# Kernel tuning notes

Measured on AMD Instinct MI355X. Metric: run time of the kernel, lower is better.

## Reference

```python
import jax, jax.numpy as jnp
import numpy as np

N = 64      # SSM state size (hidden_size)
H = 1024    # channels
L = 2048    # sequence length
BATCH = 8


def setup_inputs() -> dict:
    key = jax.random.key(0)
    ks = jax.random.split(key, 12)
    s = 1.0 / np.sqrt(N)
    n = jnp.arange(N, dtype=jnp.float32)
    return {
        "r": jax.random.normal(ks[0], (BATCH, L, H), dtype=jnp.float32),
        "B_re": jax.random.normal(ks[1], (N,), dtype=jnp.float32) * s,
        "B_im": jax.random.normal(ks[2], (N,), dtype=jnp.float32) * s,
        "C_re": jax.random.normal(ks[3], (H, N), dtype=jnp.float32) * s,
        "C_im": jax.random.normal(ks[4], (H, N), dtype=jnp.float32) * s,
        "P_re": jax.random.normal(ks[5], (N,), dtype=jnp.float32) * s,
        "P_im": jax.random.normal(ks[6], (N,), dtype=jnp.float32) * s,
        "Q_re": jax.random.normal(ks[7], (N,), dtype=jnp.float32) * s,
        "Q_im": jax.random.normal(ks[8], (N,), dtype=jnp.float32) * s,
        # HiPPO-LegS-like diagonal: negative real part for stability, imag ~ pi*n
        "diag_re": -0.5 * jnp.ones((N,), dtype=jnp.float32),
        "diag_im": jnp.pi * (n - N / 2.0),
        "step": jnp.array([1e-3], dtype=jnp.float32),
        "D": jnp.zeros((1,), dtype=jnp.float32),
    }


def _dplr_kernel(Bc, Cc, Pc, Qc, Lam, step, seq_len):
    # Standard S4 DPLR generating function evaluated at roots of unity,
    # then inverse FFT -> real convolution kernel K_c of shape (H, L).
    z = jnp.exp(-2j * jnp.pi * jnp.arange(seq_len) / seq_len).astype(jnp.complex64)  # (L,)
    g = (2.0 / step) * (1.0 - z) / (1.0 + z)                                          # (L,)
    cden = 1.0 / (g[:, None] - Lam[None, :])                                          # (L,N) Cauchy denom
    k00 = jnp.einsum('hn,ln->hl', Cc * Bc, cden)   # (H,L)
    k01 = jnp.einsum('hn,ln->hl', Cc * Pc, cden)   # (H,L)
    k10 = jnp.einsum('n,ln->l', Qc * Bc, cden)     # (L,)
    k11 = jnp.einsum('n,ln->l', Qc * Pc, cden)     # (L,)
    at_roots = (2.0 / (1.0 + z)) * (k00 - k01 * (k10 / (1.0 + k11)))  # (H,L)
    return jnp.fft.ifft(at_roots, axis=-1).real


def reference(r, B_re, B_im, C_re, C_im, P_re, P_im, Q_re, Q_im,
              diag_re, diag_im, step, D):
    step_c = jnp.maximum(step[0], 1e-6)
    Bc = B_re + 1j * B_im
    Cc = C_re + 1j * C_im
    Pc = P_re + 1j * P_im
    Qc = Q_re + 1j * Q_im
    Lam = diag_re + 1j * diag_im
    seq_len = r.shape[1]
    K = _dplr_kernel(Bc, Cc, Pc, Qc, Lam, step_c, seq_len)  # (H, L)
    # causal FFT convolution along the sequence axis
    nfft = 2 * seq_len
    Kf = jnp.fft.rfft(K, n=nfft, axis=-1)            # (H, nfft//2+1)
    uf = jnp.fft.rfft(r, n=nfft, axis=1)             # (B, nfft//2+1, H)
    h1 = jnp.fft.irfft(uf * Kf.T[None], n=nfft, axis=1)[:, :seq_len]  # (B,L,H)
    y1 = h1 + D[0] * r
    return jax.nn.gelu(y1, approximate=False)
```

## Files before the change

kernel.cpp:

```cpp
#include <hip/hip_runtime.h>
#include <math.h>

#define SSM_N 64
#define SSM_H 1024
#define SSM_L 2048
#define SSM_B 8
#define FFTN 2048
#define NT 256

#define PSWZ(a) ((a) ^ (((a) >> 4) & 15))

typedef float f2 __attribute__((ext_vector_type(2)));
static __device__ __forceinline__ f2 mkf2(float a, float b){ f2 v; v.x = a; v.y = b; return v; }

static __device__ __forceinline__ f2 cmul(f2 a, f2 b){
  return mkf2(-a.y, a.y) * mkf2(b.y, b.x) + mkf2(a.x, a.x) * b;
}
static __device__ __forceinline__ f2 cconj(f2 a){ return mkf2(a.x, -a.y); }

template<bool INV> static __device__ __forceinline__ f2 mul_mi(f2 a){
  return INV ? mkf2(-a.y, a.x) : mkf2(a.y, -a.x);
}
template<bool INV> static __device__ __forceinline__ f2 mul_w81(f2 a){
  const float r = 0.70710678118654752440f;
  return INV ? (r * mkf2(a.x - a.y, a.y + a.x)) : (r * mkf2(a.x + a.y, a.y - a.x));
}
template<bool INV> static __device__ __forceinline__ f2 mul_w83(f2 a){
  const float r = 0.70710678118654752440f;
  return INV ? (r * mkf2(-(a.x + a.y), a.x - a.y)) : (r * mkf2(a.y - a.x, -(a.x + a.y)));
}

#define W8C0 1.f
#define W8S0 0.f
#define W8C1 0.92387953251f
#define W8S1 (-0.38268343236f)
#define W8C2 0.70710678119f
#define W8S2 (-0.70710678119f)
#define W8C3 0.38268343236f
#define W8S3 (-0.92387953251f)
#define W8C4 0.f
#define W8S4 (-1.f)
#define W8C5 (-0.38268343236f)
#define W8S5 (-0.92387953251f)
#define W8C6 (-0.70710678119f)
#define W8S6 (-0.70710678119f)
#define W8C7 (-0.92387953251f)
#define W8S7 (-0.38268343236f)

template<bool INV>
static __device__ __forceinline__ void bfly8(const f2* x, f2* y)
{
  f2 t0=x[0]+x[4], t4=x[0]-x[4];
  f2 t1=x[1]+x[5], t5=x[1]-x[5];
  f2 t2=x[2]+x[6], t6=x[2]-x[6];
  f2 t3=x[3]+x[7], t7=x[3]-x[7];
  f2 b0=t0+t2, b2=t0-t2, b1=t1+t3, b3=t1-t3;
  f2 mb3 = mul_mi<INV>(b3);
  y[0]=b0+b1; y[4]=b0-b1; y[2]=b2+mb3; y[6]=b2-mb3;
  f2 v1 = mul_w81<INV>(t5), v2 = mul_mi<INV>(t6), v3 = mul_w83<INV>(t7);
  f2 a0=t4+v2, a2=t4-v2, a1=v1+v3, a3=v1-v3;
  f2 ma3 = mul_mi<INV>(a3);
  y[1]=a0+a1; y[5]=a0-a1; y[3]=a2+ma3; y[7]=a2-ma3;
}

template<bool INV>
static __device__ __forceinline__ void calc_w8(const f2* __restrict__ tw, int j, f2* w)
{
  f2 w1 = tw[j];
  if (INV) w1.y = -w1.y;
  w[1]=w1; w[2]=cmul(w1,w1); w[3]=cmul(w[2],w1); w[4]=cmul(w[2],w[2]);
  w[5]=cmul(w[3],w[2]); w[6]=cmul(w[3],w[3]); w[7]=cmul(w[4],w[3]);
}

static __device__ __forceinline__ void twstore(f2* __restrict__ dst, const f2* y, const f2* w,
                                               int base, int S)
{
  dst[PSWZ(base)]     = y[0];
  dst[PSWZ(base+S)]   = cmul(y[1],w[1]);
  dst[PSWZ(base+2*S)] = cmul(y[2],w[2]);
  dst[PSWZ(base+3*S)] = cmul(y[3],w[3]);
  dst[PSWZ(base+4*S)] = cmul(y[4],w[4]);
  dst[PSWZ(base+5*S)] = cmul(y[5],w[5]);
  dst[PSWZ(base+6*S)] = cmul(y[6],w[6]);
  dst[PSWZ(base+7*S)] = cmul(y[7],w[7]);
}

template<bool INV>
static __device__ __forceinline__ void bfly8_store(f2* __restrict__ dst, const f2* __restrict__ tw,
                                                   f2* x, int j, int base, int S)
{
  f2 y[8]; bfly8<INV>(x, y);
  f2 w[8]; calc_w8<INV>(tw, j, w);
  twstore(dst, y, w, base, S);
}

template<bool INV, int S>
static __device__ __forceinline__ void stage8_mid_ip(f2* __restrict__ buf, const f2* __restrict__ tw,
                                                     int t, int st)
{
  f2 x[8];
  #pragma unroll
  for (int q = 0; q < 8; ++q) x[q] = buf[st + 256*q];
  __syncthreads();
  int i = t & (S-1);
  int j = t - i;
  bfly8_store<INV>(buf, tw, x, j, i + j*8, S);
  __syncthreads();
}

template<bool INV>
static __device__ __forceinline__ void stage4f_ip(f2* __restrict__ buf, int st)
{
  f2 xr[2][4];
  #pragma unroll
  for (int hh = 0; hh < 2; ++hh) {
    const f2* sp = buf + st + 256*hh;
    xr[hh][0]=sp[0]; xr[hh][1]=sp[512]; xr[hh][2]=sp[1024]; xr[hh][3]=sp[1536];
  }
  __syncthreads();
  #pragma unroll
  for (int hh = 0; hh < 2; ++hh) {
    f2* wp = buf + st + 256*hh;
    f2 a0=xr[hh][0]+xr[hh][2], a2=xr[hh][0]-xr[hh][2];
    f2 a1=xr[hh][1]+xr[hh][3], a3=xr[hh][1]-xr[hh][3];
    f2 m = mul_mi<INV>(a3);
    wp[0]    = a0+a1;
    wp[512]  = a2+m;
    wp[1024] = a0-a1;
    wp[1536] = a2-m;
  }
  __syncthreads();
}

template<bool INV>
static __device__ __forceinline__ void stage4f_reg(const f2* __restrict__ src, f2* out, int st)
{
  #pragma unroll
  for (int hh = 0; hh < 2; ++hh) {
    const f2* sp = src + st + 256*hh;
    f2 x0=sp[0], x1=sp[512], x2=sp[1024], x3=sp[1536];
    f2 a0=x0+x2, a2=x0-x2, a1=x1+x3, a3=x1-x3;
    f2 m = mul_mi<INV>(a3);
    out[hh]   = a0+a1;
    out[hh+2] = a2+m;
    out[hh+4] = a0-a1;
    out[hh+6] = a2-m;
  }
}

static __device__ __forceinline__ f2 init_tw(f2* tw, int t)
{
  float s, c;
  sincosf(-6.2831853071795864769f * (float)t / (float)FFTN, &s, &c);
  f2 v = mkf2(c, s);
  tw[t] = v;
  return v;
}

__global__ __launch_bounds__(256) void kprep(
    const float* __restrict__ B_re, const float* __restrict__ B_im,
    const float* __restrict__ P_re, const float* __restrict__ P_im,
    const float* __restrict__ Q_re, const float* __restrict__ Q_im,
    const float* __restrict__ diag_re, const float* __restrict__ diag_im,
    const float* __restrict__ step,
    f2* __restrict__ cdenT, f2* __restrict__ f2v, f2* __restrict__ facv)
{
  int gid = blockIdx.x * 256 + threadIdx.x;
  int l = gid >> 3, s = gid & 7;
  double stepc = (double)step[0]; if (stepc < 1e-6) stepc = 1e-6;
  double ang = -2.0 * 3.14159265358979323846 * (double)l / (double)SSM_L;
  double zr = cos(ang), zi = sin(ang);
  double dr = 1.0 + zr, di = zi;
  double nr = 1.0 - zr, ni = -zi;
  double den = dr*dr + di*di;
  double i2s = 2.0 / stepc;
  double gr = i2s * (nr*dr + ni*di) / den;
  double gi = i2s * (ni*dr - nr*di) / den;
  double k10r=0.0, k10i=0.0, k11r=0.0, k11i=0.0;
  #pragma unroll
  for (int q = 0; q < 8; ++q) {
    int n = s*8 + q;
    double ar = gr - (double)diag_re[n];
    double ai = gi - (double)diag_im[n];
    double d2 = ar*ar + ai*ai;
    double cr = ar/d2, ci = -ai/d2;
    cdenT[n*SSM_L + l] = mkf2((float)cr, (float)ci);
    double qr = (double)Q_re[n], qi = (double)Q_im[n];
    double br = (double)B_re[n], bi = (double)B_im[n];
    double pr = (double)P_re[n], pi = (double)P_im[n];
    double qbr = qr*br - qi*bi, qbi = qr*bi + qi*br;
    double qpr = qr*pr - qi*pi, qpi = qr*pi + qi*pr;
    k10r += qbr*cr - qbi*ci; k10i += qbr*ci + qbi*cr;
    k11r += qpr*cr - qpi*ci; k11i += qpr*ci + qpi*cr;
  }
  #pragma unroll
  for (int off = 1; off < 8; off <<= 1) {
    k10r += __shfl_xor(k10r, off);
    k10i += __shfl_xor(k10i, off);
    k11r += __shfl_xor(k11r, off);
    k11i += __shfl_xor(k11i, off);
  }
  if (s == 0) {
    f2v[l] = mkf2((float)(2.0*dr/den), (float)(-2.0*di/den));
    double er = 1.0 + k11r, ei = k11i;
    double ed = er*er + ei*ei;
    facv[l] = mkf2((float)((k10r*er + k10i*ei)/ed), (float)((k10i*er - k10r*ei)/ed));
  }
}

__global__ __launch_bounds__(NT, 3) void kmid(
    const float* __restrict__ r, float* __restrict__ rT,
    const float* __restrict__ C_re, const float* __restrict__ C_im,
    const float* __restrict__ B_re, const float* __restrict__ B_im,
    const float* __restrict__ P_re, const float* __restrict__ P_im,
    const f2* __restrict__ cdenT, const f2* __restrict__ f2v, const f2* __restrict__ facv,
    float4* __restrict__ PQg)
{
  __shared__ f2 smem[FFTN + 256];
  int bid = blockIdx.x;
  int t = threadIdx.x;
  int nk = bid / 5, rem = bid - nk*5;
  if (rem != 0) {
    float (*til)[65] = (float (*)[65])smem;
    int td = nk*4 + rem - 1;
    int tx = t & 15, ty = t >> 4;
    int h0 = (td & 15) * 64, l0 = ((td >> 4) & 31) * 64, b = td >> 9;
    const float4* s4 = (const float4*)(r + ((size_t)b*SSM_L + l0)*SSM_H + h0);
    #pragma unroll
    for (int i = 0; i < 4; ++i) {
      int lr = ty + 16*i;
      float4 v = s4[(size_t)lr*(SSM_H/4) + tx];
      til[lr][4*tx+0]=v.x; til[lr][4*tx+1]=v.y; til[lr][4*tx+2]=v.z; til[lr][4*tx+3]=v.w;
    }
    __syncthreads();
    float4* d4 = (float4*)(rT + ((size_t)b*SSM_H + h0)*SSM_L + l0);
    #pragma unroll
    for (int i = 0; i < 4; ++i) {
      int hr = ty + 16*i;
      float4 w;
      w.x = til[4*tx+0][hr]; w.y = til[4*tx+1][hr];
      w.z = til[4*tx+2][hr]; w.w = til[4*tx+3][hr];
      d4[(size_t)hr*(SSM_L/4) + tx] = w;
    }
    return;
  }
  f2* buf = smem;
  f2* tw  = smem + FFTN;
  int st = PSWZ(t);
  int h = nk;
  init_tw(tw, t);
  f2* cbs = buf;
  if (t < 128) {
    int n = t & 63;
    f2 cc = mkf2(C_re[h*SSM_N + n], C_im[h*SSM_N + n]);
    cbs[t] = (t < 64) ? cmul(cc, mkf2(B_re[n], B_im[n]))
                      : cmul(cc, mkf2(P_re[n], P_im[n]));
  }
  __syncthreads();
  f2 k00[8], k01[8];
  #pragma unroll
  for (int i = 0; i < 8; ++i) { k00[i] = mkf2(0.f,0.f); k01[i] = mkf2(0.f,0.f); }
  for (int n = 0; n < SSM_N; ++n) {
    f2 cb = cbs[n], cp = cbs[64 + n];
    #pragma unroll
    for (int i = 0; i < 8; ++i) {
      f2 cd = cdenT[n*SSM_L + t + i*NT];
      k00[i] = k00[i] + cmul(cb, cd);
      k01[i] = k01[i] + cmul(cp, cd);
    }
  }
  __syncthreads();
  f2 ar[8];
  #pragma unroll
  for (int i = 0; i < 8; ++i) {
    int l = t + i*NT;
    ar[i] = cmul(f2v[l], k00[i] - cmul(k01[i], facv[l]));
    buf[PSWZ(l)] = ar[i];
  }
  __syncthreads();
  f2 ebin[4], e2048 = mkf2(0.f, 0.f);
  #pragma unroll
  for (int i = 0; i < 4; ++i) {
    int m = t + i*NT;
    if (m == 0) {
      ebin[0] = mkf2(buf[0].x, 0.f);
      e2048   = mkf2(buf[PSWZ(FFTN/2)].x, 0.f);
    } else {
      ebin[i] = 0.5f * (buf[PSWZ(m)] + cconj(buf[PSWZ(FFTN - m)]));
    }
  }
  __syncthreads();
  bfly8_store<true>(buf, tw, ar, t, t*8, 1);
  __syncthreads();
  stage8_mid_ip<true, 8>(buf, tw, t, st);
  stage8_mid_ip<true, 64>(buf, tw, t, st);
  f2 kr[8];
  stage4f_reg<true>(buf, kr, st);
  {
    float sbb, cbb;
    sincosf(-3.14159265358979f * (float)t / (float)FFTN, &sbb, &cbb);
    f2 cbase = mkf2(cbb, sbb);
    const float Wc8[8] = {W8C0,W8C1,W8C2,W8C3,W8C4,W8C5,W8C6,W8C7};
    const float Ws8[8] = {W8S0,W8S1,W8S2,W8S3,W8S4,W8S5,W8S6,W8S7};
    const float scale = 1.0f / (float)FFTN;
    #pragma unroll
    for (int q = 0; q < 8; ++q) {
      f2 tq = cmul(cbase, mkf2(Wc8[q], Ws8[q]));
      kr[q] = (kr[q].x * scale) * tq;
    }
  }
  __syncthreads();
  bfly8_store<false>(buf, tw, kr, t, t*8, 1);
  __syncthreads();
  stage8_mid_ip<false, 8>(buf, tw, t, st);
  stage8_mid_ip<false, 64>(buf, tw, t, st);
  {
    f2 xr[2][4];
    #pragma unroll
    for (int hh = 0; hh < 2; ++hh) {
      const f2* sp = buf + st + 256*hh;
      xr[hh][0]=sp[0]; xr[hh][1]=sp[512]; xr[hh][2]=sp[1024]; xr[hh][3]=sp[1536];
    }
    __syncthreads();
    #pragma unroll
    for (int hh = 0; hh < 2; ++hh) {
      f2* wp = buf + st + 256*hh;
      f2 a0=xr[hh][0]+xr[hh][2], a2=xr[hh][0]-xr[hh][2];
      f2 a1=xr[hh][1]+xr[hh][3], a3=xr[hh][1]-xr[hh][3];
      f2 m = mul_mi<false>(a3);
      wp[0]   = a0+a1;
      wp[512] = a2+m;
    }
    #pragma unroll
    for (int i = 0; i < 4; ++i) {
      int m = t + 256*i;
      f2 v = ebin[i];
      if (m == 0) v = e2048;
      buf[1024 + m] = v;
    }
  }
  __syncthreads();
  f2 u = tw[t];
  const float q4 = 1.0f / 4096.0f;
  const f2 c1 = mkf2(0.99999882345170176f, -0.00153398018628477f);
  f2 base_odd = cmul(c1, u);
  const float Wc8[8] = {W8C0,W8C1,W8C2,W8C3,W8C4,W8C5,W8C6,W8C7};
  const float Ws8[8] = {W8S0,W8S1,W8S2,W8S3,W8S4,W8S5,W8S6,W8S7};
  float4* pqrow = PQg + (size_t)h * FFTN;
  #pragma unroll
  for (int i = 0; i < 4; ++i) {
    int m = t + 256*i;
    f2 Ka = ebin[i];
    f2 Kb = buf[1024 + ((1024 - m) & 1023)];
    f2 ee = cmul(u, mkf2(Wc8[2*i], Ws8[2*i]));
    float cv = ee.x, sv = -ee.y;
    float am = q4*(1.f - sv), ap = q4*(1.f + sv), cq = q4*cv;
    f2 P = mkf2(Ka.x*am + Kb.x*ap, Ka.y*am - Kb.y*ap);
    f2 dd = mkf2(Ka.x - Kb.x, Ka.y + Kb.y);
    pqrow[2*m] = make_float4(P.x, P.y, -dd.y*cq, dd.x*cq);
    f2 Ko = buf[PSWZ(m)];
    f2 Kp = buf[PSWZ(1023 - m)];
    f2 eo = cmul(base_odd, mkf2(Wc8[2*i], Ws8[2*i]));
    cv = eo.x; sv = -eo.y;
    am = q4*(1.f - sv); ap = q4*(1.f + sv); cq = q4*cv;
    f2 P2 = mkf2(Ko.x*am + Kp.x*ap, Ko.y*am - Kp.y*ap);
    f2 d2 = mkf2(Ko.x - Kp.x, Ko.y + Kp.y);
    pqrow[2*m+1] = make_float4(P2.x, P2.y, -d2.y*cq, d2.x*cq);
  }
}

__global__ __launch_bounds__(NT, 4) void kconv(float* __restrict__ rT,
                                               const float4* __restrict__ PQg,
                                               const float* __restrict__ Dp)
{
  __shared__ f2 buf[FFTN];
  __shared__ f2 tw[256];
  int t = threadIdx.x, st = PSWZ(t);
  int xc = blockIdx.x & 7, y = blockIdx.x >> 3;
  int h = xc * 128 + (y >> 3);
  int b = y & 7;
  float Dv = Dp[0];
  init_tw(tw, t);
  float* rrow = rT + ((size_t)b*SSM_H + h) * SSM_L;
  const f2* r2 = (const f2*)rrow;
  f2 rv[4];
  #pragma unroll
  for (int i = 0; i < 4; ++i) rv[i] = r2[t + i*NT];
  {
    f2 xx[8];
    #pragma unroll
    for (int q = 0; q < 4; ++q) { xx[q] = rv[q]; xx[q+4] = mkf2(0.f, 0.f); }
    bfly8_store<false>(buf, tw, xx, t, t*8, 1);
  }
  __syncthreads();
  stage8_mid_ip<false, 8>(buf, tw, t, st);
  stage8_mid_ip<false, 64>(buf, tw, t, st);
  const float4* pqrow = PQg + (size_t)h * FFTN;
  float4 pq[8];
  #pragma unroll
  for (int i = 0; i < 8; ++i) pq[i] = pqrow[t + i*NT];
  stage4f_ip<false>(buf, st);
  {
    f2 xx[8];
    #pragma unroll
    for (int i = 0; i < 8; ++i) {
      int k = t + i*NT;
      int kk = (FFTN - k) & (FFTN - 1);
      f2 Ck  = buf[st + i*NT];
      f2 Ckk = buf[PSWZ(kk)];
      xx[i] = cmul(mkf2(pq[i].x, pq[i].y), Ck) + cmul(mkf2(pq[i].z, pq[i].w), cconj(Ckk));
    }
    __syncthreads();
    bfly8_store<true>(buf, tw, xx, t, t*8, 1);
  }
  __syncthreads();
  stage8_mid_ip<true, 8>(buf, tw, t, st);
  stage8_mid_ip<true, 64>(buf, tw, t, st);
  f2* o2 = (f2*)rrow;
  #pragma unroll
  for (int hh = 0; hh < 2; ++hh) {
    const f2* sp = buf + st + 256*hh;
    f2 x0=sp[0], x1=sp[512], x2=sp[1024], x3=sp[1536];
    f2 a0=x0+x2, a2=x0-x2, a1=x1+x3, a3=x1-x3;
    f2 mm = mul_mi<true>(a3);
    f2 y0 = a0+a1, y1 = a2+mm;
    f2 rA = rv[hh], rB = rv[hh+2];
    o2[t + 256*hh]       = mkf2(y0.x + Dv*rA.x, y0.y + Dv*rA.y);
    o2[t + 256*hh + 512] = mkf2(y1.x + Dv*rB.x, y1.y + Dv*rB.y);
  }
}

__global__ __launch_bounds__(256) void ktback(const float* __restrict__ yT, float* __restrict__ out)
{
  __shared__ float til[64][65];
  int t = threadIdx.x, tx = t & 15, ty = t >> 4;
  int h0 = blockIdx.x * 64, l0 = blockIdx.y * 64, b = blockIdx.z;
  const float4* s4 = (const float4*)(yT + ((size_t)b*SSM_H + h0)*SSM_L + l0);
  #pragma unroll
  for (int i = 0; i < 4; ++i) {
    int hr = ty + 16*i;
    float4 v = s4[(size_t)hr*(SSM_L/4) + tx];
    til[hr][4*tx+0]=v.x; til[hr][4*tx+1]=v.y; til[hr][4*tx+2]=v.z; til[hr][4*tx+3]=v.w;
  }
  __syncthreads();
  float4* d4 = (float4*)(out + ((size_t)b*SSM_L + l0)*SSM_H + h0);
  #pragma unroll
  for (int i = 0; i < 4; ++i) {
    int lr = ty + 16*i;
    float4 w;
    float x0 = til[4*tx+0][lr], x1 = til[4*tx+1][lr];
    float x2 = til[4*tx+2][lr], x3 = til[4*tx+3][lr];
    w.x = 0.5f * x0 * (1.0f + erff(x0 * 0.70710678118654752f));
    w.y = 0.5f * x1 * (1.0f + erff(x1 * 0.70710678118654752f));
    w.z = 0.5f * x2 * (1.0f + erff(x2 * 0.70710678118654752f));
    w.w = 0.5f * x3 * (1.0f + erff(x3 * 0.70710678118654752f));
    d4[(size_t)lr*(SSM_H/4) + tx] = w;
  }
}

extern "C" void kernel_launch(void* const* d_in, const int* in_sizes, int n_in,
                              void* d_out, int out_size, void* d_ws, size_t ws_size,
                              hipStream_t stream)
{
  const float* r       = (const float*)d_in[0];
  const float* B_re    = (const float*)d_in[1];
  const float* B_im    = (const float*)d_in[2];
  const float* C_re    = (const float*)d_in[3];
  const float* C_im    = (const float*)d_in[4];
  const float* P_re    = (const float*)d_in[5];
  const float* P_im    = (const float*)d_in[6];
  const float* Q_re    = (const float*)d_in[7];
  const float* Q_im    = (const float*)d_in[8];
  const float* diag_re = (const float*)d_in[9];
  const float* diag_im = (const float*)d_in[10];
  const float* step    = (const float*)d_in[11];
  const float* Dp      = (const float*)d_in[12];
  float* out = (float*)d_out;

  char* p = (char*)d_ws;
  float* rT  = (float*)p;  p += (size_t)SSM_B*SSM_H*SSM_L*sizeof(float);
  f2* cdenT  = (f2*)p;     p += (size_t)SSM_N*SSM_L*sizeof(f2);
  f2* f2v    = (f2*)p;     p += (size_t)SSM_L*sizeof(f2);
  f2* facv   = (f2*)p;     p += (size_t)SSM_L*sizeof(f2);
  float4* PQ = (float4*)p; p += (size_t)SSM_H*FFTN*sizeof(float4);

  kprep<<<64, 256, 0, stream>>>(B_re, B_im, P_re, P_im, Q_re, Q_im,
                                diag_re, diag_im, step, cdenT, f2v, facv);
  kmid<<<5120, NT, 0, stream>>>(r, rT, C_re, C_im, B_re, B_im, P_re, P_im,
                                cdenT, f2v, facv, PQ);
  kconv<<<SSM_B*SSM_H, NT, 0, stream>>>(rT, PQ, Dp);
  ktback<<<dim3(SSM_H/64, SSM_L/64, SSM_B), 256, 0, stream>>>(rT, out);
}
```

Baseline: 308.4 us.

## Split Cauchy contraction into register-blocked kernel and move transpose into prep kernel

The DPLR Cauchy contraction moves out of the FFT kernel into a dedicated kernel. Each thread there handles one sequence position for eight channels, so each cdenT load is reused across eight channels and the next row is prefetched. The input transpose moves into the prep kernel so it runs alongside the cdenT computation, and the FFT kernel now only reads the precomputed at-roots values. The cost is an extra launch and a round trip of the intermediate through the output buffer, used as scratch.

Measured after the change: 282.2 us. 1.09x faster.

```diff
diff --git a/kernel.cpp b/kernel.cpp
--- a/kernel.cpp
+++ b/kernel.cpp
@@ -158,6 +158,7 @@
 }
 
 __global__ __launch_bounds__(256) void kprep(
+    const float* __restrict__ r, float* __restrict__ rT,
     const float* __restrict__ B_re, const float* __restrict__ B_im,
     const float* __restrict__ P_re, const float* __restrict__ P_im,
     const float* __restrict__ Q_re, const float* __restrict__ Q_im,
@@ -165,66 +166,12 @@
     const float* __restrict__ step,
     f2* __restrict__ cdenT, f2* __restrict__ f2v, f2* __restrict__ facv)
 {
-  int gid = blockIdx.x * 256 + threadIdx.x;
-  int l = gid >> 3, s = gid & 7;
-  double stepc = (double)step[0]; if (stepc < 1e-6) stepc = 1e-6;
-  double ang = -2.0 * 3.14159265358979323846 * (double)l / (double)SSM_L;
-  double zr = cos(ang), zi = sin(ang);
-  double dr = 1.0 + zr, di = zi;
-  double nr = 1.0 - zr, ni = -zi;
-  double den = dr*dr + di*di;
-  double i2s = 2.0 / stepc;
-  double gr = i2s * (nr*dr + ni*di) / den;
-  double gi = i2s * (ni*dr - nr*di) / den;
-  double k10r=0.0, k10i=0.0, k11r=0.0, k11i=0.0;
-  #pragma unroll
-  for (int q = 0; q < 8; ++q) {
-    int n = s*8 + q;
-    double ar = gr - (double)diag_re[n];
-    double ai = gi - (double)diag_im[n];
-    double d2 = ar*ar + ai*ai;
-    double cr = ar/d2, ci = -ai/d2;
-    cdenT[n*SSM_L + l] = mkf2((float)cr, (float)ci);
-    double qr = (double)Q_re[n], qi = (double)Q_im[n];
-    double br = (double)B_re[n], bi = (double)B_im[n];
-    double pr = (double)P_re[n], pi = (double)P_im[n];
-    double qbr = qr*br - qi*bi, qbi = qr*bi + qi*br;
-    double qpr = qr*pr - qi*pi, qpi = qr*pi + qi*pr;
-    k10r += qbr*cr - qbi*ci; k10i += qbr*ci + qbi*cr;
-    k11r += qpr*cr - qpi*ci; k11i += qpr*ci + qpi*cr;
-  }
-  #pragma unroll
-  for (int off = 1; off < 8; off <<= 1) {
-    k10r += __shfl_xor(k10r, off);
-    k10i += __shfl_xor(k10i, off);
-    k11r += __shfl_xor(k11r, off);
-    k11i += __shfl_xor(k11i, off);
-  }
-  if (s == 0) {
-    f2v[l] = mkf2((float)(2.0*dr/den), (float)(-2.0*di/den));
-    double er = 1.0 + k11r, ei = k11i;
-    double ed = er*er + ei*ei;
-    facv[l] = mkf2((float)((k10r*er + k10i*ei)/ed), (float)((k10i*er - k10r*ei)/ed));
-  }
-}
-
-__global__ __launch_bounds__(NT, 3) void kmid(
-    const float* __restrict__ r, float* __restrict__ rT,
-    const float* __restrict__ C_re, const float* __restrict__ C_im,
-    const float* __restrict__ B_re, const float* __restrict__ B_im,
-    const float* __restrict__ P_re, const float* __restrict__ P_im,
-    const f2* __restrict__ cdenT, const f2* __restrict__ f2v, const f2* __restrict__ facv,
-    float4* __restrict__ PQg)
-{
-  __shared__ f2 smem[FFTN + 256];
+  __shared__ float til[64][65];
   int bid = blockIdx.x;
   int t = threadIdx.x;
-  int nk = bid / 5, rem = bid - nk*5;
-  if (rem != 0) {
-    float (*til)[65] = (float (*)[65])smem;
-    int td = nk*4 + rem - 1;
+  if (bid < 4096) {
     int tx = t & 15, ty = t >> 4;
-    int h0 = (td & 15) * 64, l0 = ((td >> 4) & 31) * 64, b = td >> 9;
+    int h0 = (bid & 15) * 64, l0 = ((bid >> 4) & 31) * 64, b = bid >> 9;
     const float4* s4 = (const float4*)(r + ((size_t)b*SSM_L + l0)*SSM_H + h0);
     #pragma unroll
     for (int i = 0; i < 4; ++i) {
@@ -242,39 +189,101 @@
       w.z = til[4*tx+2][hr]; w.w = til[4*tx+3][hr];
       d4[(size_t)hr*(SSM_L/4) + tx] = w;
     }
-    return;
-  }
-  f2* buf = smem;
-  f2* tw  = smem + FFTN;
-  int st = PSWZ(t);
-  int h = nk;
+  } else {
+    int gid = (bid - 4096) * 256 + t;
+    int l = gid >> 3, s = gid & 7;
+    double stepc = (double)step[0]; if (stepc < 1e-6) stepc = 1e-6;
+    double ang = -2.0 * 3.14159265358979323846 * (double)l / (double)SSM_L;
+    double zr = cos(ang), zi = sin(ang);
+    double dr = 1.0 + zr, di = zi;
+    double nr = 1.0 - zr, ni = -zi;
+    double den = dr*dr + di*di;
+    double i2s = 2.0 / stepc;
+    double gr = i2s * (nr*dr + ni*di) / den;
+    double gi = i2s * (ni*dr - nr*di) / den;
+    double k10r=0.0, k10i=0.0, k11r=0.0, k11i=0.0;
+    #pragma unroll
+    for (int q = 0; q < 8; ++q) {
+      int n = s*8 + q;
+      double ar = gr - (double)diag_re[n];
+      double ai = gi - (double)diag_im[n];
+      double d2 = ar*ar + ai*ai;
+      double cr = ar/d2, ci = -ai/d2;
+      cdenT[n*SSM_L + l] = mkf2((float)cr, (float)ci);
+      double qr = (double)Q_re[n], qi = (double)Q_im[n];
+      double br = (double)B_re[n], bi = (double)B_im[n];
+      double pr = (double)P_re[n], pi = (double)P_im[n];
+      double qbr = qr*br - qi*bi, qbi = qr*bi + qi*br;
+      double qpr = qr*pr - qi*pi, qpi = qr*pi + qi*pr;
+      k10r += qbr*cr - qbi*ci; k10i += qbr*ci + qbi*cr;
+      k11r += qpr*cr - qpi*ci; k11i += qpr*ci + qpi*cr;
+    }
+    #pragma unroll
+    for (int off = 1; off < 8; off <<= 1) {
+      k10r += __shfl_xor(k10r, off);
+      k10i += __shfl_xor(k10i, off);
+      k11r += __shfl_xor(k11r, off);
+      k11i += __shfl_xor(k11i, off);
+    }
+    if (s == 0) {
+      f2v[l] = mkf2((float)(2.0*dr/den), (float)(-2.0*di/den));
+      double er = 1.0 + k11r, ei = k11i;
+      double ed = er*er + ei*ei;
+      facv[l] = mkf2((float)((k10r*er + k10i*ei)/ed), (float)((k10i*er - k10r*ei)/ed));
+    }
+  }
+}
+
+__global__ __launch_bounds__(256, 2) void kcontr(
+    const float* __restrict__ C_re, const float* __restrict__ C_im,
+    const float* __restrict__ B_re, const float* __restrict__ B_im,
+    const float* __restrict__ P_re, const float* __restrict__ P_im,
+    const f2* __restrict__ cdenT, const f2* __restrict__ f2v, const f2* __restrict__ facv,
+    f2* __restrict__ arT)
+{
+  __shared__ f2 cbs[1024];
+  int t = threadIdx.x;
+  int bh = blockIdx.x >> 3, lt = blockIdx.x & 7;
+  int h0 = bh * 8, l = lt * 256 + t;
+  for (int i = t; i < 1024; i += 256) {
+    int sel = i >> 9, c = (i >> 6) & 7, n = i & 63;
+    f2 cc = mkf2(C_re[(h0+c)*SSM_N + n], C_im[(h0+c)*SSM_N + n]);
+    cbs[i] = sel ? cmul(cc, mkf2(P_re[n], P_im[n]))
+                 : cmul(cc, mkf2(B_re[n], B_im[n]));
+  }
+  __syncthreads();
+  f2 k0[8], k1[8];
+  #pragma unroll
+  for (int c = 0; c < 8; ++c) { k0[c] = mkf2(0.f,0.f); k1[c] = mkf2(0.f,0.f); }
+  f2 cd = cdenT[l];
+  for (int n = 0; n < SSM_N; ++n) {
+    f2 cdn = cdenT[((n+1)&63)*SSM_L + l];
+    #pragma unroll
+    for (int c = 0; c < 8; ++c) {
+      k0[c] = k0[c] + cmul(cbs[c*64 + n], cd);
+      k1[c] = k1[c] + cmul(cbs[512 + c*64 + n], cd);
+    }
+    cd = cdn;
+  }
+  f2 fv = f2v[l], fc = facv[l];
+  #pragma unroll
+  for (int c = 0; c < 8; ++c)
+    arT[(size_t)(h0+c)*SSM_L + l] = cmul(fv, k0[c] - cmul(k1[c], fc));
+}
+
+__global__ __launch_bounds__(NT, 4) void kfft(
+    const f2* __restrict__ arT, float4* __restrict__ PQg)
+{
+  __shared__ f2 buf[FFTN];
+  __shared__ f2 tw[256];
+  int t = threadIdx.x, st = PSWZ(t);
+  int h = blockIdx.x;
   init_tw(tw, t);
-  f2* cbs = buf;
-  if (t < 128) {
-    int n = t & 63;
-    f2 cc = mkf2(C_re[h*SSM_N + n], C_im[h*SSM_N + n]);
-    cbs[t] = (t < 64) ? cmul(cc, mkf2(B_re[n], B_im[n]))
-                      : cmul(cc, mkf2(P_re[n], P_im[n]));
-  }
-  __syncthreads();
-  f2 k00[8], k01[8];
-  #pragma unroll
-  for (int i = 0; i < 8; ++i) { k00[i] = mkf2(0.f,0.f); k01[i] = mkf2(0.f,0.f); }
-  for (int n = 0; n < SSM_N; ++n) {
-    f2 cb = cbs[n], cp = cbs[64 + n];
-    #pragma unroll
-    for (int i = 0; i < 8; ++i) {
-      f2 cd = cdenT[n*SSM_L + t + i*NT];
-      k00[i] = k00[i] + cmul(cb, cd);
-      k01[i] = k01[i] + cmul(cp, cd);
-    }
-  }
-  __syncthreads();
   f2 ar[8];
   #pragma unroll
   for (int i = 0; i < 8; ++i) {
     int l = t + i*NT;
-    ar[i] = cmul(f2v[l], k00[i] - cmul(k01[i], facv[l]));
+    ar[i] = arT[(size_t)h*SSM_L + l];
     buf[PSWZ(l)] = ar[i];
   }
   __syncthreads();
@@ -483,11 +492,13 @@
   f2* f2v    = (f2*)p;     p += (size_t)SSM_L*sizeof(f2);
   f2* facv   = (f2*)p;     p += (size_t)SSM_L*sizeof(f2);
   float4* PQ = (float4*)p; p += (size_t)SSM_H*FFTN*sizeof(float4);
-
-  kprep<<<64, 256, 0, stream>>>(B_re, B_im, P_re, P_im, Q_re, Q_im,
-                                diag_re, diag_im, step, cdenT, f2v, facv);
-  kmid<<<5120, NT, 0, stream>>>(r, rT, C_re, C_im, B_re, B_im, P_re, P_im,
-                                cdenT, f2v, facv, PQ);
+  f2* arT    = (f2*)out;
+
+  kprep<<<4096 + 64, 256, 0, stream>>>(r, rT, B_re, B_im, P_re, P_im, Q_re, Q_im,
+                                       diag_re, diag_im, step, cdenT, f2v, facv);
+  kcontr<<<1024, 256, 0, stream>>>(C_re, C_im, B_re, B_im, P_re, P_im,
+                                   cdenT, f2v, facv, arT);
+  kfft<<<SSM_H, NT, 0, stream>>>(arT, PQ);
   kconv<<<SSM_B*SSM_H, NT, 0, stream>>>(rT, PQ, Dp);
   ktback<<<dim3(SSM_H/64, SSM_L/64, SSM_B), 256, 0, stream>>>(rT, out);
 }
```
